# Optimization experiments

Hardware: AMD Instinct MI355X
Metric: run time of the kernel (lower is better)

The kernel has to match this reference:

```python
import jax, jax.numpy as jnp
import numpy as np

N = 150000   # total supergraph nodes (entities+events+chains)
D = 128      # embed_size
H = 4        # attention heads
DH = D // H  # head dim
E = 300000   # edges per layer
L = 4        # layer_specs length
A = 8        # edge attr dim
T = 10       # num_edge_type
TIME_SCALE = 24.0
SLOPE = 0.2  # negative_slope


def setup_inputs() -> dict:
    key = jax.random.key(0)
    ks = jax.random.split(key, 16)
    nrm = lambda k, s, sc=1.0: jax.random.normal(k, s, dtype=jnp.float32) * sc
    return {
        'x': nrm(ks[0], (N, D), 0.1),
        'Wq': nrm(ks[1], (L, D, D), D ** -0.5),
        'Wk': nrm(ks[2], (L, D, D), D ** -0.5),
        'Wv': nrm(ks[3], (L, D, D), D ** -0.5),
        'Wskip': nrm(ks[4], (L, D, D), D ** -0.5),
        'Wa': nrm(ks[5], (L, A, D), 0.1),
        'time_w': nrm(ks[6], (D,)),
        'time_b': nrm(ks[7], (D,), 0.1),
        'dist_w': nrm(ks[8], (D,)),
        'dist_b': nrm(ks[9], (D,), 0.1),
        'type_table': nrm(ks[10], (T, D), 0.1),
        'bn_gamma': jnp.ones((L, D), jnp.float32),
        'bn_beta': jnp.zeros((L, D), jnp.float32),
        'beta': jnp.full((L,), 0.5, jnp.float32),
        'edge_attr': jax.random.uniform(ks[11], (L, E, A), dtype=jnp.float32),
        'edge_dt': jax.random.uniform(ks[12], (L, E), dtype=jnp.float32) * TIME_SCALE,
        'edge_ds': jax.random.uniform(ks[13], (L, E), dtype=jnp.float32) * 10.0,
        'edge_index': jax.random.randint(ks[14], (L, 2, E), 0, N),
        'edge_type': jax.random.randint(ks[15], (L, E), 0, T),
    }


def _layer(x, Wq, Wk, Wv, Wskip, Wa, time_w, time_b, dist_w, dist_b,
           type_table, gamma, bvec, beta, attr, dt, ds, ei, et):
    n = x.shape[0]
    src, dst = ei[0], ei[1]
    # continuous time / distance encoders: cos basis (TimeEncoder / 'time' DistanceEncoder)
    te = jnp.cos((dt / TIME_SCALE)[:, None] * time_w + time_b)   # [E,D]
    de = jnp.cos(ds[:, None] * dist_w + dist_b)                  # [E,D]
    # 'add' edge/time fusion: attr MLP + time + dist + edge-type embeddings
    edge_feat = attr @ Wa + te + de + type_table[et]             # [E,D]
    kv_in = x[src] + edge_feat                                   # gather + fuse
    q = (x @ Wq).reshape(n, H, DH)[dst]                          # [E,H,DH]
    k = (kv_in @ Wk).reshape(-1, H, DH)
    v = (kv_in @ Wv).reshape(-1, H, DH)
    logits = (q * k).sum(-1) * (DH ** -0.5)                      # [E,H]
    logits = jnp.where(logits >= 0, logits, SLOPE * logits)      # leaky_relu(negative_slope)
    # segment softmax over incoming edges of each destination node
    m = jax.ops.segment_max(logits, dst, num_segments=n)
    a = jnp.exp(logits - m[dst])
    denom = jax.ops.segment_sum(a, dst, num_segments=n)
    a = a / denom[dst]
    agg = jax.ops.segment_sum(a[..., None] * v, dst, num_segments=n).reshape(n, D)
    # beta-weighted residual (learn_beta) with skip projection
    out = beta * (x @ Wskip) + (1.0 - beta) * agg
    # BatchNorm1d (training-mode batch stats) + ReLU
    mu = out.mean(0)
    var = out.var(0)
    out = (out - mu) * jax.lax.rsqrt(var + 1e-5) * gamma + bvec
    return jax.nn.relu(out)


def reference(x, Wq, Wk, Wv, Wskip, Wa, time_w, time_b, dist_w, dist_b,
              type_table, bn_gamma, bn_beta, beta, edge_attr, edge_dt,
              edge_ds, edge_index, edge_type):
    for l in range(L):  # entity2event, event2event, event2chain (time filter), chain2chain
        x = _layer(x, Wq[l], Wk[l], Wv[l], Wskip[l], Wa[l],
                   time_w, time_b, dist_w, dist_b, type_table,
                   bn_gamma[l], bn_beta[l], beta[l],
                   edge_attr[l], edge_dt[l], edge_ds[l],
                   edge_index[l], edge_type[l])
    return x
```

## Files before the change

kernel.cpp:

```cpp
#include <hip/hip_runtime.h>

typedef unsigned int u32;
typedef unsigned short u16;
typedef short bf16x8 __attribute__((ext_vector_type(8)));
typedef float f32x4 __attribute__((ext_vector_type(4)));

#define N_NODES 150000
#define E_EDGES 300000
#define L_CNT   151552
#define ETILES  9375
#define NTILES  4688
#define KVBLKS  37500

__device__ __forceinline__ float blo(u32 u){ return __uint_as_float(u << 16); }
__device__ __forceinline__ float bhi(u32 u){ return __uint_as_float(u & 0xffff0000u); }
__device__ __forceinline__ float b2f(u16 h){ return __uint_as_float(((u32)h) << 16); }
__device__ __forceinline__ u16 f2bf(float f){
  u32 u = __float_as_uint(f);
  return (u16)((u + 0x7fffu + ((u >> 16) & 1u)) >> 16);
}
__device__ __forceinline__ u32 pack2(float a, float b){
  return (u32)f2bf(a) | ((u32)f2bf(b) << 16);
}

__device__ __forceinline__ f32x4 mfma16(bf16x8 a, bf16x8 b, f32x4 c){
  return __builtin_amdgcn_mfma_f32_16x16x32_bf16(a, b, c, 0, 0, 0);
}

__device__ __forceinline__ int opsw(int r, int k){ return (r * 128 + k) ^ ((r & 7) << 3); }
__device__ __forceinline__ int csw(int r, int n){ return (r * 128 + n) ^ (((r >> 2) & 3) << 3); }

__global__ __launch_bounds__(256)
void k_wt(const float* __restrict__ Wq, const float* __restrict__ Wk,
          const float* __restrict__ Wv, const float* __restrict__ Ws,
          u16* __restrict__ Wt)
{
  const int m = blockIdx.x;
  const float* src = (m < 4 ? Wq : m < 8 ? Wk : m < 12 ? Wv : Ws)
                     + (size_t)(m & 3) * 16384;
  u16* dst = Wt + (size_t)m * 16384;
  const int t = threadIdx.x;
  for (int i = 0; i < 16; ++i) {
    int idx = i * 256 + t;
    int n = idx >> 5;
    int k4 = (idx & 31) << 2;
    ushort4 o;
    o.x = f2bf(src[(k4 + 0) * 128 + n]);
    o.y = f2bf(src[(k4 + 1) * 128 + n]);
    o.z = f2bf(src[(k4 + 2) * 128 + n]);
    o.w = f2bf(src[(k4 + 3) * 128 + n]);
    *(ushort4*)(dst + n * 128 + k4) = o;
  }
}


__global__ __launch_bounds__(256)
void k_hist(const int* __restrict__ eidx, int* __restrict__ counts)
{
  const int l = blockIdx.y;
  const int e = blockIdx.x * 256 + threadIdx.x;
  if (e < E_EDGES) {
    int dst = eidx[(size_t)l * 2 * E_EDGES + E_EDGES + e];
    atomicAdd(&counts[(size_t)l * L_CNT + dst], 1);
  }
}

__global__ __launch_bounds__(256)
void k_scan1(const int* __restrict__ counts, int* __restrict__ rowptr,
             int* __restrict__ bsum)
{
  __shared__ int sh[256];
  const int b = blockIdx.x, l = blockIdx.y;
  const int t = threadIdx.x;
  const int* c = counts + (size_t)l * L_CNT + b * 2048;
  int* rp = rowptr + (size_t)l * L_CNT + b * 2048;
  int v[8]; int s = 0;
  #pragma unroll
  for (int j = 0; j < 8; ++j) { v[j] = c[t * 8 + j]; s += v[j]; }
  sh[t] = s; __syncthreads();
  for (int off = 1; off < 256; off <<= 1) {
    int x = (t >= off) ? sh[t - off] : 0;
    __syncthreads();
    sh[t] += x;
    __syncthreads();
  }
  int excl = (t == 0) ? 0 : sh[t - 1];
  if (t == 255) bsum[l * 128 + b] = sh[255];
  int run = excl;
  #pragma unroll
  for (int j = 0; j < 8; ++j) { rp[t * 8 + j] = run; run += v[j]; }
}

__global__ __launch_bounds__(128)
void k_scan2(int* __restrict__ bsum)
{
  __shared__ int sh[128];
  const int l = blockIdx.x, t = threadIdx.x;
  int v = (t < 74) ? bsum[l * 128 + t] : 0;
  sh[t] = v; __syncthreads();
  for (int off = 1; off < 128; off <<= 1) {
    int x = (t >= off) ? sh[t - off] : 0;
    __syncthreads();
    sh[t] += x;
    __syncthreads();
  }
  int excl = (t == 0) ? 0 : sh[t - 1];
  if (t < 74) bsum[l * 128 + t] = excl;
}

__global__ __launch_bounds__(256)
void k_scan3(int* __restrict__ rowptr, int* __restrict__ tmp,
             const int* __restrict__ bsum)
{
  const int l = blockIdx.y;
  const int q = blockIdx.x * 256 + threadIdx.x;
  int v = rowptr[(size_t)l * L_CNT + q] + bsum[l * 128 + (q >> 11)];
  rowptr[(size_t)l * L_CNT + q] = v;
  tmp[(size_t)l * L_CNT + q] = v;
}

__global__ __launch_bounds__(256)
void k_scatter(const int* __restrict__ srcP, const int* __restrict__ dstP,
               const int* __restrict__ etP, const float* __restrict__ dtP,
               const float* __restrict__ dsP, const float* __restrict__ attrP,
               int* __restrict__ tmpL, u32* __restrict__ meta)
{
  const int e = blockIdx.x * 256 + threadIdx.x;
  if (e < E_EDGES) {
    int dst = dstP[e];
    int pos = atomicAdd(&tmpL[dst], 1);
    int src = srcP[e];
    int et  = etP[e];
    float dtn = dtP[e] * (1.0f / 24.0f);
    float dsv = dsP[e];
    float4 aA = *(const float4*)(attrP + (size_t)e * 8);
    float4 aB = *(const float4*)(attrP + (size_t)e * 8 + 4);
    uint4 r0, r1;
    r0.x = (u32)src;
    r0.y = (u32)dst | ((u32)et << 20);
    r0.z = __float_as_uint(dtn);
    r0.w = __float_as_uint(dsv);
    r1.x = pack2(aA.x, aA.y); r1.y = pack2(aA.z, aA.w);
    r1.z = pack2(aB.x, aB.y); r1.w = pack2(aB.z, aB.w);
    u32* mp = meta + (size_t)pos * 8;
    *(uint4*)mp = r0;
    *(uint4*)(mp + 4) = r1;
  }
}

__global__ __launch_bounds__(128)
void bn_stats(const float* __restrict__ colsum, const float* __restrict__ colsumsq,
              const float* __restrict__ gamma, const float* __restrict__ bvec,
              float* __restrict__ scsh)
{
  const int d = threadIdx.x;
  const float invN = 1.f / 150000.f;
  float mu = colsum[d] * invN;
  float var = colsumsq[d] * invN - mu * mu;
  float sc = gamma[d] * rsqrtf(var + 1e-5f);
  scsh[d] = sc;
  scsh[128 + d] = bvec[d] - mu * sc;
}


template<int XF32, int BN>
__global__ __launch_bounds__(128, 2)
void prep(const void* __restrict__ xg, const u16* __restrict__ WtQ,
          const u16* __restrict__ WtS, const float* __restrict__ scsh,
          u16* __restrict__ Qo, u16* __restrict__ So,
          const float* __restrict__ Wa, const float* __restrict__ tw,
          const float* __restrict__ tb, const float* __restrict__ dw,
          const float* __restrict__ db, const float* __restrict__ ttab,
          const u32* __restrict__ meta, u16* __restrict__ kvV)
{
  __shared__ __align__(16) u16 As[4160];
  __shared__ __align__(16) u16 Bs[4160];
  const int t = threadIdx.x;

  if (blockIdx.x < NTILES) {
    const int w = t >> 6, lane = t & 63;
    const int lr = lane & 15, hi = lane >> 4;
    const int row0 = blockIdx.x * 32;
    const int nr = min(32, N_NODES - row0);
    const u16* Wt = w ? WtS : WtQ;
    u16* C = w ? So : Qo;

    bf16x8 wt[8][4];
    #pragma unroll
    for (int nb = 0; nb < 8; ++nb)
      #pragma unroll
      for (int ks = 0; ks < 4; ++ks)
        wt[nb][ks] = *(const bf16x8*)(Wt + (nb * 16 + lr) * 128 + ks * 32 + hi * 8);

    #pragma unroll
    for (int i = 0; i < 4; ++i) {
      int idx = i * 128 + t;
      int r = idx >> 4, c8 = (idx & 15) << 3;
      if (r < nr) {
        if (XF32) {
          float4 vA = *(const float4*)((const float*)xg + (size_t)(row0 + r) * 128 + c8);
          float4 vB = *(const float4*)((const float*)xg + (size_t)(row0 + r) * 128 + c8 + 4);
          uint4 o;
          o.x = pack2(vA.x, vA.y); o.y = pack2(vA.z, vA.w);
          o.z = pack2(vB.x, vB.y); o.w = pack2(vB.z, vB.w);
          *(uint4*)(As + opsw(r, c8)) = o;
        } else {
          uint4 v = *(const uint4*)((const u16*)xg + (size_t)(row0 + r) * 128 + c8);
          if (BN) {
            float4 scA = *(const float4*)(scsh + c8);
            float4 scB = *(const float4*)(scsh + c8 + 4);
            float4 shA = *(const float4*)(scsh + 128 + c8);
            float4 shB = *(const float4*)(scsh + 128 + c8 + 4);
            float e0v = fmaxf(fmaf(blo(v.x), scA.x, shA.x), 0.f);
            float e1v = fmaxf(fmaf(bhi(v.x), scA.y, shA.y), 0.f);
            float e2v = fmaxf(fmaf(blo(v.y), scA.z, shA.z), 0.f);
            float e3v = fmaxf(fmaf(bhi(v.y), scA.w, shA.w), 0.f);
            float e4v = fmaxf(fmaf(blo(v.z), scB.x, shB.x), 0.f);
            float e5v = fmaxf(fmaf(bhi(v.z), scB.y, shB.y), 0.f);
            float e6v = fmaxf(fmaf(blo(v.w), scB.z, shB.z), 0.f);
            float e7v = fmaxf(fmaf(bhi(v.w), scB.w, shB.w), 0.f);
            v.x = pack2(e0v, e1v); v.y = pack2(e2v, e3v);
            v.z = pack2(e4v, e5v); v.w = pack2(e6v, e7v);
          }
          *(uint4*)(As + opsw(r, c8)) = v;
        }
      } else {
        *(uint4*)(As + opsw(r, c8)) = make_uint4(0, 0, 0, 0);
      }
    }
    __syncthreads();

    f32x4 acc[2][8];
    #pragma unroll
    for (int a = 0; a < 2; ++a)
      #pragma unroll
      for (int b = 0; b < 8; ++b) {
        acc[a][b][0] = 0.f; acc[a][b][1] = 0.f;
        acc[a][b][2] = 0.f; acc[a][b][3] = 0.f;
      }
    #pragma unroll
    for (int ks = 0; ks < 4; ++ks) {
      const int kb = ks * 32 + hi * 8;
      bf16x8 a0 = *(const bf16x8*)(As + opsw(lr, kb));
      bf16x8 a1 = *(const bf16x8*)(As + opsw(16 + lr, kb));
      #pragma unroll
      for (int nb = 0; nb < 8; ++nb) {
        acc[0][nb] = mfma16(a0, wt[nb][ks], acc[0][nb]);
        acc[1][nb] = mfma16(a1, wt[nb][ks], acc[1][nb]);
      }
    }
    __syncthreads();

    u16* Cs = w ? Bs : As;
    const int g4 = hi << 2;
    #pragma unroll
    for (int mt = 0; mt < 2; ++mt)
      #pragma unroll
      for (int nt = 0; nt < 8; ++nt)
        #pragma unroll
        for (int j = 0; j < 4; ++j)
          Cs[csw(mt * 16 + g4 + j, nt * 16 + lr)] = f2bf(acc[mt][nt][j]);
    #pragma unroll
    for (int i = 0; i < 8; ++i) {
      int idx = i * 64 + lane;
      int r = idx >> 4, n8 = (idx & 15) << 3;
      if (r < nr) {
        uint4 v = *(const uint4*)(Cs + csw(r, n8));
        *(uint4*)(C + (size_t)(row0 + r) * 128 + n8) = v;
      }
    }
  } else {
    const int idx = (blockIdx.x - NTILES) * 128 + t;
    const int e = idx >> 4;
    const int c8 = (idx & 15) << 3;
    const u32* mp = meta + (size_t)e * 8;
    uint4 m0 = *(const uint4*)mp;
    uint4 m1 = *(const uint4*)(mp + 4);
    const int src = (int)m0.x;
    const int et = (int)(m0.y >> 20);
    const float dtn = __uint_as_float(m0.z);
    const float dss = __uint_as_float(m0.w);
    float aa[8] = { blo(m1.x), bhi(m1.x), blo(m1.y), bhi(m1.y),
                    blo(m1.z), bhi(m1.z), blo(m1.w), bhi(m1.w) };
    const float4 twA = *(const float4*)(tw + c8);
    const float4 twB = *(const float4*)(tw + c8 + 4);
    const float4 tbA = *(const float4*)(tb + c8);
    const float4 tbB = *(const float4*)(tb + c8 + 4);
    const float4 dwA = *(const float4*)(dw + c8);
    const float4 dwB = *(const float4*)(dw + c8 + 4);
    const float4 dbA = *(const float4*)(db + c8);
    const float4 dbB = *(const float4*)(db + c8 + 4);
    const float4 ttA = *(const float4*)(ttab + et * 128 + c8);
    const float4 ttB = *(const float4*)(ttab + et * 128 + c8 + 4);
    float f[8];
    f[0] = __cosf(fmaf(dtn, twA.x, tbA.x)) + __cosf(fmaf(dss, dwA.x, dbA.x)) + ttA.x;
    f[1] = __cosf(fmaf(dtn, twA.y, tbA.y)) + __cosf(fmaf(dss, dwA.y, dbA.y)) + ttA.y;
    f[2] = __cosf(fmaf(dtn, twA.z, tbA.z)) + __cosf(fmaf(dss, dwA.z, dbA.z)) + ttA.z;
    f[3] = __cosf(fmaf(dtn, twA.w, tbA.w)) + __cosf(fmaf(dss, dwA.w, dbA.w)) + ttA.w;
    f[4] = __cosf(fmaf(dtn, twB.x, tbB.x)) + __cosf(fmaf(dss, dwB.x, dbB.x)) + ttB.x;
    f[5] = __cosf(fmaf(dtn, twB.y, tbB.y)) + __cosf(fmaf(dss, dwB.y, dbB.y)) + ttB.y;
    f[6] = __cosf(fmaf(dtn, twB.z, tbB.z)) + __cosf(fmaf(dss, dwB.z, dbB.z)) + ttB.z;
    f[7] = __cosf(fmaf(dtn, twB.w, tbB.w)) + __cosf(fmaf(dss, dwB.w, dbB.w)) + ttB.w;
    #pragma unroll
    for (int a = 0; a < 8; ++a) {
      float4 wA = *(const float4*)(Wa + a * 128 + c8);
      float4 wB = *(const float4*)(Wa + a * 128 + c8 + 4);
      f[0] = fmaf(aa[a], wA.x, f[0]);
      f[1] = fmaf(aa[a], wA.y, f[1]);
      f[2] = fmaf(aa[a], wA.z, f[2]);
      f[3] = fmaf(aa[a], wA.w, f[3]);
      f[4] = fmaf(aa[a], wB.x, f[4]);
      f[5] = fmaf(aa[a], wB.y, f[5]);
      f[6] = fmaf(aa[a], wB.z, f[6]);
      f[7] = fmaf(aa[a], wB.w, f[7]);
    }
    float xv[8];
    if (XF32) {
      float4 xA = *(const float4*)((const float*)xg + (size_t)src * 128 + c8);
      float4 xB = *(const float4*)((const float*)xg + (size_t)src * 128 + c8 + 4);
      xv[0] = xA.x; xv[1] = xA.y; xv[2] = xA.z; xv[3] = xA.w;
      xv[4] = xB.x; xv[5] = xB.y; xv[6] = xB.z; xv[7] = xB.w;
    } else {
      uint4 xr = *(const uint4*)((const u16*)xg + (size_t)src * 128 + c8);
      xv[0] = blo(xr.x); xv[1] = bhi(xr.x); xv[2] = blo(xr.y); xv[3] = bhi(xr.y);
      xv[4] = blo(xr.z); xv[5] = bhi(xr.z); xv[6] = blo(xr.w); xv[7] = bhi(xr.w);
    }
    if (BN) {
      float4 scA = *(const float4*)(scsh + c8);
      float4 scB = *(const float4*)(scsh + c8 + 4);
      float4 shA = *(const float4*)(scsh + 128 + c8);
      float4 shB = *(const float4*)(scsh + 128 + c8 + 4);
      xv[0] = fmaxf(fmaf(xv[0], scA.x, shA.x), 0.f);
      xv[1] = fmaxf(fmaf(xv[1], scA.y, shA.y), 0.f);
      xv[2] = fmaxf(fmaf(xv[2], scA.z, shA.z), 0.f);
      xv[3] = fmaxf(fmaf(xv[3], scA.w, shA.w), 0.f);
      xv[4] = fmaxf(fmaf(xv[4], scB.x, shB.x), 0.f);
      xv[5] = fmaxf(fmaf(xv[5], scB.y, shB.y), 0.f);
      xv[6] = fmaxf(fmaf(xv[6], scB.z, shB.z), 0.f);
      xv[7] = fmaxf(fmaf(xv[7], scB.w, shB.w), 0.f);
    }
    uint4 o;
    o.x = pack2(xv[0] + f[0], xv[1] + f[1]);
    o.y = pack2(xv[2] + f[2], xv[3] + f[3]);
    o.z = pack2(xv[4] + f[4], xv[5] + f[5]);
    o.w = pack2(xv[6] + f[6], xv[7] + f[7]);
    *(uint4*)(kvV + (size_t)e * 128 + c8) = o;
  }
}


__global__ __launch_bounds__(128, 2)
void edge_kv(const u16* __restrict__ WtK, const u16* __restrict__ WtV,
             const u32* __restrict__ meta, const u16* __restrict__ Qb,
             u16* __restrict__ kvV, float* __restrict__ logits)
{
  __shared__ __align__(16) u16 KVs[4160];
  __shared__ __align__(16) u16 Qs[4160];
  __shared__ int dstSh[32];
  const int t = threadIdx.x;
  const int w = t >> 6, lane = t & 63;
  const int lr = lane & 15, hi = lane >> 4;
  const int e0 = blockIdx.x * 32;
  const u16* Wt = w ? WtV : WtK;

  bf16x8 wt[8][4];
  #pragma unroll
  for (int nb = 0; nb < 8; ++nb)
    #pragma unroll
    for (int ks = 0; ks < 4; ++ks)
      wt[nb][ks] = *(const bf16x8*)(Wt + (nb * 16 + lr) * 128 + ks * 32 + hi * 8);

  if (w == 0) {
    #pragma unroll
    for (int i = 0; i < 8; ++i) {
      int idx = i * 64 + lane;
      int r = idx >> 4, c8 = (idx & 15) << 3;
      uint4 v = *(const uint4*)(kvV + (size_t)(e0 + r) * 128 + c8);
      *(uint4*)(KVs + opsw(r, c8)) = v;
    }
  } else {
    if (lane < 32)
      dstSh[lane] = (int)(meta[(size_t)(e0 + lane) * 8 + 1] & 0xFFFFFu);
    #pragma unroll
    for (int i = 0; i < 8; ++i) {
      int idx = i * 64 + lane;
      int r = idx >> 4, c8 = (idx & 15) << 3;
      int qrow = dstSh[r];
      uint4 qv = *(const uint4*)(Qb + (size_t)qrow * 128 + c8);
      *(uint4*)(Qs + opsw(r, c8)) = qv;
    }
  }
  __syncthreads();

  if (w == 0) {
    #pragma unroll
    for (int eb = 0; eb < 2; ++eb) {
      f32x4 kacc[8];
      #pragma unroll
      for (int b = 0; b < 8; ++b) {
        kacc[b][0] = 0.f; kacc[b][1] = 0.f; kacc[b][2] = 0.f; kacc[b][3] = 0.f;
      }
      #pragma unroll
      for (int ks = 0; ks < 4; ++ks) {
        bf16x8 ef = *(const bf16x8*)(KVs + opsw(eb * 16 + lr, ks * 32 + hi * 8));
        #pragma unroll
        for (int nb = 0; nb < 8; ++nb)
          kacc[nb] = mfma16(wt[nb][ks], ef, kacc[nb]);
      }
      const int el = eb * 16 + lr;
      float hs[4] = {0.f, 0.f, 0.f, 0.f};
      #pragma unroll
      for (int nb = 0; nb < 8; ++nb) {
        ushort4 q = *(const ushort4*)(Qs + opsw(el, nb * 16 + hi * 4));
        hs[nb >> 1] += b2f(q.x) * kacc[nb][0] + b2f(q.y) * kacc[nb][1]
                     + b2f(q.z) * kacc[nb][2] + b2f(q.w) * kacc[nb][3];
      }
      #pragma unroll
      for (int h = 0; h < 4; ++h) {
        hs[h] += __shfl_xor(hs[h], 16, 64);
        hs[h] += __shfl_xor(hs[h], 32, 64);
        hs[h] *= 0.17677669529663687f;
        hs[h] = (hs[h] >= 0.f) ? hs[h] : 0.2f * hs[h];
      }
      if (lane < 16)
        *(float4*)(logits + (size_t)(e0 + el) * 4) = make_float4(hs[0], hs[1], hs[2], hs[3]);
    }
    __syncthreads();
  } else {
    f32x4 vacc[2][8];
    #pragma unroll
    for (int a = 0; a < 2; ++a)
      #pragma unroll
      for (int b = 0; b < 8; ++b) {
        vacc[a][b][0] = 0.f; vacc[a][b][1] = 0.f;
        vacc[a][b][2] = 0.f; vacc[a][b][3] = 0.f;
      }
    #pragma unroll
    for (int ks = 0; ks < 4; ++ks) {
      const int kb = ks * 32 + hi * 8;
      bf16x8 a0 = *(const bf16x8*)(KVs + opsw(lr, kb));
      bf16x8 a1 = *(const bf16x8*)(KVs + opsw(16 + lr, kb));
      #pragma unroll
      for (int nb = 0; nb < 8; ++nb) {
        vacc[0][nb] = mfma16(a0, wt[nb][ks], vacc[0][nb]);
        vacc[1][nb] = mfma16(a1, wt[nb][ks], vacc[1][nb]);
      }
    }
    __syncthreads();
    const int g4 = hi << 2;
    #pragma unroll
    for (int mt = 0; mt < 2; ++mt)
      #pragma unroll
      for (int nt = 0; nt < 8; ++nt)
        #pragma unroll
        for (int j = 0; j < 4; ++j)
          Qs[csw(mt * 16 + g4 + j, nt * 16 + lr)] = f2bf(vacc[mt][nt][j]);
    #pragma unroll
    for (int i = 0; i < 8; ++i) {
      int idx = i * 64 + lane;
      int r = idx >> 4, n8 = (idx & 15) << 3;
      uint4 v = *(const uint4*)(Qs + csw(r, n8));
      *(uint4*)(kvV + (size_t)(e0 + r) * 128 + n8) = v;
    }
  }
}

template<int PREBF16>
__global__ __launch_bounds__(256)
void node_agg(const u16* __restrict__ Vs, const float* __restrict__ logits,
              const int* __restrict__ rowptr, const u16* __restrict__ S,
              const float* __restrict__ betaP, float* __restrict__ pre,
              u16* __restrict__ preb, float* __restrict__ colsum,
              float* __restrict__ colsumsq)
{
  __shared__ float red[1024];
  const int t = threadIdx.x;
  const int g = t >> 5;
  const int lane = t & 31;
  const int d0 = lane * 4;
  const int h = lane >> 3;
  const float beta = *betaP;
  const float omb = 1.f - beta;
  float s4[4] = {0.f, 0.f, 0.f, 0.f};
  float q4[4] = {0.f, 0.f, 0.f, 0.f};
  for (int rep = 0; rep < 16; ++rep) {
    int n = blockIdx.x * 128 + rep * 8 + g;
    if (n < N_NODES) {
      int rs = rowptr[n], re = rowptr[n + 1];
      float m = -1e30f;
      for (int i = rs; i < re; ++i)
        m = fmaxf(m, logits[(size_t)i * 4 + h]);
      float den = 0.f;
      float a0 = 0.f, a1 = 0.f, a2 = 0.f, a3 = 0.f;
      for (int i = rs; i < re; ++i) {
        float wgt = __expf(logits[(size_t)i * 4 + h] - m);
        den += wgt;
        ushort4 v = *(const ushort4*)(Vs + (size_t)i * 128 + d0);
        a0 = fmaf(wgt, b2f(v.x), a0);
        a1 = fmaf(wgt, b2f(v.y), a1);
        a2 = fmaf(wgt, b2f(v.z), a2);
        a3 = fmaf(wgt, b2f(v.w), a3);
      }
      float inv = (den > 0.f) ? (omb / den) : 0.f;
      ushort4 sv = *(const ushort4*)(S + (size_t)n * 128 + d0);
      float p0 = fmaf(beta, b2f(sv.x), a0 * inv);
      float p1 = fmaf(beta, b2f(sv.y), a1 * inv);
      float p2 = fmaf(beta, b2f(sv.z), a2 * inv);
      float p3 = fmaf(beta, b2f(sv.w), a3 * inv);
      if (PREBF16) {
        ushort4 o;
        o.x = f2bf(p0); o.y = f2bf(p1); o.z = f2bf(p2); o.w = f2bf(p3);
        *(ushort4*)(preb + (size_t)n * 128 + d0) = o;
      } else {
        *(float4*)(pre + (size_t)n * 128 + d0) = make_float4(p0, p1, p2, p3);
      }
      s4[0] += p0; s4[1] += p1; s4[2] += p2; s4[3] += p3;
      q4[0] += p0 * p0; q4[1] += p1 * p1; q4[2] += p2 * p2; q4[3] += p3 * p3;
    }
  }
  *(float4*)(&red[g * 128 + d0]) = make_float4(s4[0], s4[1], s4[2], s4[3]);
  __syncthreads();
  if (t < 128) {
    float tot = 0.f;
    #pragma unroll
    for (int gg = 0; gg < 8; ++gg) tot += red[gg * 128 + t];
    atomicAdd(&colsum[t], tot);
  }
  __syncthreads();
  *(float4*)(&red[g * 128 + d0]) = make_float4(q4[0], q4[1], q4[2], q4[3]);
  __syncthreads();
  if (t < 128) {
    float tot = 0.f;
    #pragma unroll
    for (int gg = 0; gg < 8; ++gg) tot += red[gg * 128 + t];
    atomicAdd(&colsumsq[t], tot);
  }
}

__global__ __launch_bounds__(256)
void bn_apply(const float* __restrict__ pre, const float* __restrict__ colsum,
              const float* __restrict__ colsumsq, const float* __restrict__ gamma,
              const float* __restrict__ bvec, float* __restrict__ outf)
{
  const int idx = blockIdx.x * 256 + threadIdx.x;
  const int n = idx >> 5;
  const int d0 = (idx & 31) * 4;
  const float invN = 1.f / 150000.f;
  float4 p = *(const float4*)(pre + (size_t)n * 128 + d0);
  float4 cs = *(const float4*)(colsum + d0);
  float4 cq = *(const float4*)(colsumsq + d0);
  float4 gm = *(const float4*)(gamma + d0);
  float4 bv = *(const float4*)(bvec + d0);
  float mu, var, y;
  mu = cs.x * invN; var = cq.x * invN - mu * mu;
  y = (p.x - mu) * rsqrtf(var + 1e-5f) * gm.x + bv.x; p.x = fmaxf(y, 0.f);
  mu = cs.y * invN; var = cq.y * invN - mu * mu;
  y = (p.y - mu) * rsqrtf(var + 1e-5f) * gm.y + bv.y; p.y = fmaxf(y, 0.f);
  mu = cs.z * invN; var = cq.z * invN - mu * mu;
  y = (p.z - mu) * rsqrtf(var + 1e-5f) * gm.z + bv.z; p.z = fmaxf(y, 0.f);
  mu = cs.w * invN; var = cq.w * invN - mu * mu;
  y = (p.w - mu) * rsqrtf(var + 1e-5f) * gm.w + bv.w; p.w = fmaxf(y, 0.f);
  *(float4*)(outf + (size_t)n * 128 + d0) = p;
}

extern "C" void kernel_launch(void* const* d_in, const int* in_sizes, int n_in,
                              void* d_out, int out_size, void* d_ws, size_t ws_size,
                              hipStream_t stream)
{
  const float* x0    = (const float*)d_in[0];
  const float* Wq    = (const float*)d_in[1];
  const float* Wk    = (const float*)d_in[2];
  const float* Wv    = (const float*)d_in[3];
  const float* Wsk   = (const float*)d_in[4];
  const float* Wa    = (const float*)d_in[5];
  const float* tw    = (const float*)d_in[6];
  const float* tb    = (const float*)d_in[7];
  const float* dw    = (const float*)d_in[8];
  const float* db    = (const float*)d_in[9];
  const float* ttab  = (const float*)d_in[10];
  const float* gam   = (const float*)d_in[11];
  const float* bet   = (const float*)d_in[12];
  const float* betaP = (const float*)d_in[13];
  const float* attr  = (const float*)d_in[14];
  const float* dt    = (const float*)d_in[15];
  const float* dsv   = (const float*)d_in[16];
  const int*   eidx  = (const int*)d_in[17];
  const int*   etyp  = (const int*)d_in[18];

  char* p = (char*)d_ws;
  u16* xbf  = (u16*)p;       p += 38400000;
  u16* Q    = (u16*)p;       p += 38400000;
  u16* S    = (u16*)p;       p += 38400000;
  u16* kvV  = (u16*)p;       p += 76800000;
  float* logits = (float*)p; p += 4800000;
  int* rowptr = (int*)p;     p += 4 * L_CNT * 4;
  int* tmp    = (int*)p;     p += 4 * L_CNT * 4;
  int* bsum   = (int*)p;     p += 4 * 128 * 4;
  float* colsum   = (float*)p; p += 512;
  float* colsumsq = (float*)p; p += 512;
  float* scsh     = (float*)p; p += 1024;
  u16* Wt = (u16*)p;         p += 16 * 16384 * 2;
  u32* meta = (u32*)p;       p += (size_t)E_EDGES * 32;

  float* pre = (float*)d_out;

  k_wt<<<16, 256, 0, stream>>>(Wq, Wk, Wv, Wsk, Wt);
  hipMemsetAsync(tmp, 0, 4 * L_CNT * 4, stream);
  k_hist<<<dim3(1172, 4), 256, 0, stream>>>(eidx, tmp);
  k_scan1<<<dim3(74, 4), 256, 0, stream>>>(tmp, rowptr, bsum);
  k_scan2<<<4, 128, 0, stream>>>(bsum);
  k_scan3<<<dim3(592, 4), 256, 0, stream>>>(rowptr, tmp, bsum);

  for (int l = 0; l < 4; ++l) {
    const int* srcA = eidx + (size_t)l * 600000;
    const int* dstA = srcA + 300000;
    const int* rpl = rowptr + (size_t)l * L_CNT;
    const u16* WtQl = Wt + (size_t)l * 16384;
    const u16* WtKl = Wt + (size_t)(4 + l) * 16384;
    const u16* WtVl = Wt + (size_t)(8 + l) * 16384;
    const u16* WtSl = Wt + (size_t)(12 + l) * 16384;
    const float* Wal = Wa + (size_t)l * 1024;

    k_scatter<<<1172, 256, 0, stream>>>(
        srcA, dstA, etyp + (size_t)l * 300000, dt + (size_t)l * 300000,
        dsv + (size_t)l * 300000, attr + (size_t)l * 2400000,
        tmp + (size_t)l * L_CNT, meta);

    hipMemsetAsync(colsum, 0, 1024, stream);

    if (l == 0) {
      prep<1, 0><<<NTILES + KVBLKS, 128, 0, stream>>>(
          (const void*)x0, WtQl, WtSl, scsh, Q, S,
          Wal, tw, tb, dw, db, ttab, meta, kvV);
    } else {
      prep<0, 1><<<NTILES + KVBLKS, 128, 0, stream>>>(
          (const void*)xbf, WtQl, WtSl, scsh, Q, S,
          Wal, tw, tb, dw, db, ttab, meta, kvV);
    }

    edge_kv<<<ETILES, 128, 0, stream>>>(WtKl, WtVl, meta, Q, kvV, logits);

    if (l < 3) {
      node_agg<1><<<1172, 256, 0, stream>>>(kvV, logits, rpl, S, betaP + l,
                                            nullptr, xbf, colsum, colsumsq);
      bn_stats<<<1, 128, 0, stream>>>(colsum, colsumsq, gam + (size_t)l * 128,
                                      bet + (size_t)l * 128, scsh);
    } else {
      node_agg<0><<<1172, 256, 0, stream>>>(kvV, logits, rpl, S, betaP + l,
                                            pre, nullptr, colsum, colsumsq);
      bn_apply<<<18750, 256, 0, stream>>>(pre, colsum, colsumsq,
                                          gam + (size_t)l * 128,
                                          bet + (size_t)l * 128, (float*)d_out);
    }
  }
}
```

Measured before the change: 1.429 ms.

## Fuse next-layer edge scatter into prep kernel and interleave GEMM with edge blocks

Removes the per-layer k_scatter launch by appending extra blocks to the prep kernel that build the next layer's CSR-sorted edge metadata into a double-buffered meta array. Only the first layer's scatter is launched separately, before the loop. Prep block indexing now interleaves one node-GEMM tile with every eight edge-feature blocks, so MFMA-heavy and memory-heavy blocks run concurrently instead of in two phases. The cost is a second metadata buffer and a heavier, more branchy prep grid.

```diff
diff --git a/kernel.cpp b/kernel.cpp
--- a/kernel.cpp
+++ b/kernel.cpp
@@ -11,6 +11,8 @@
 #define ETILES  9375
 #define NTILES  4688
 #define KVBLKS  37500
+#define PREPB   42192
+#define SCATB   2344
 
 __device__ __forceinline__ float blo(u32 u){ return __uint_as_float(u << 16); }
 __device__ __forceinline__ float bhi(u32 u){ return __uint_as_float(u & 0xffff0000u); }
@@ -119,6 +121,32 @@
   tmp[(size_t)l * L_CNT + q] = v;
 }
 
+__device__ __forceinline__ void scatter_one(
+    int e, const int* __restrict__ srcP, const int* __restrict__ dstP,
+    const int* __restrict__ etP, const float* __restrict__ dtP,
+    const float* __restrict__ dsP, const float* __restrict__ attrP,
+    int* __restrict__ tmpL, u32* __restrict__ meta)
+{
+  int dst = dstP[e];
+  int pos = atomicAdd(&tmpL[dst], 1);
+  int src = srcP[e];
+  int et  = etP[e];
+  float dtn = dtP[e] * (1.0f / 24.0f);
+  float dsv = dsP[e];
+  float4 aA = *(const float4*)(attrP + (size_t)e * 8);
+  float4 aB = *(const float4*)(attrP + (size_t)e * 8 + 4);
+  uint4 r0, r1;
+  r0.x = (u32)src;
+  r0.y = (u32)dst | ((u32)et << 20);
+  r0.z = __float_as_uint(dtn);
+  r0.w = __float_as_uint(dsv);
+  r1.x = pack2(aA.x, aA.y); r1.y = pack2(aA.z, aA.w);
+  r1.z = pack2(aB.x, aB.y); r1.w = pack2(aB.z, aB.w);
+  u32* mp = meta + (size_t)pos * 8;
+  *(uint4*)mp = r0;
+  *(uint4*)(mp + 4) = r1;
+}
+
 __global__ __launch_bounds__(256)
 void k_scatter(const int* __restrict__ srcP, const int* __restrict__ dstP,
                const int* __restrict__ etP, const float* __restrict__ dtP,
@@ -126,26 +154,8 @@
                int* __restrict__ tmpL, u32* __restrict__ meta)
 {
   const int e = blockIdx.x * 256 + threadIdx.x;
-  if (e < E_EDGES) {
-    int dst = dstP[e];
-    int pos = atomicAdd(&tmpL[dst], 1);
-    int src = srcP[e];
-    int et  = etP[e];
-    float dtn = dtP[e] * (1.0f / 24.0f);
-    float dsv = dsP[e];
-    float4 aA = *(const float4*)(attrP + (size_t)e * 8);
-    float4 aB = *(const float4*)(attrP + (size_t)e * 8 + 4);
-    uint4 r0, r1;
-    r0.x = (u32)src;
-    r0.y = (u32)dst | ((u32)et << 20);
-    r0.z = __float_as_uint(dtn);
-    r0.w = __float_as_uint(dsv);
-    r1.x = pack2(aA.x, aA.y); r1.y = pack2(aA.z, aA.w);
-    r1.z = pack2(aB.x, aB.y); r1.w = pack2(aB.z, aB.w);
-    u32* mp = meta + (size_t)pos * 8;
-    *(uint4*)mp = r0;
-    *(uint4*)(mp + 4) = r1;
-  }
+  if (e < E_EDGES)
+    scatter_one(e, srcP, dstP, etP, dtP, dsP, attrP, tmpL, meta);
 }
 
 __global__ __launch_bounds__(128)
@@ -171,16 +181,28 @@
           const float* __restrict__ Wa, const float* __restrict__ tw,
           const float* __restrict__ tb, const float* __restrict__ dw,
           const float* __restrict__ db, const float* __restrict__ ttab,
-          const u32* __restrict__ meta, u16* __restrict__ kvV)
+          const u32* __restrict__ meta, u16* __restrict__ kvV,
+          const int* __restrict__ srcN, const int* __restrict__ dstN,
+          const int* __restrict__ etN, const float* __restrict__ dtN,
+          const float* __restrict__ dsN, const float* __restrict__ attrN,
+          int* __restrict__ tmpN, u32* __restrict__ metaN)
 {
   __shared__ __align__(16) u16 As[4160];
   __shared__ __align__(16) u16 Bs[4160];
+  const int b = blockIdx.x;
   const int t = threadIdx.x;
 
-  if (blockIdx.x < NTILES) {
+  if (b >= PREPB) {
+    int e = (b - PREPB) * 128 + t;
+    if (metaN != nullptr && e < E_EDGES)
+      scatter_one(e, srcN, dstN, etN, dtN, dsN, attrN, tmpN, metaN);
+    return;
+  }
+
+  if (b % 9 == 0) {
     const int w = t >> 6, lane = t & 63;
     const int lr = lane & 15, hi = lane >> 4;
-    const int row0 = blockIdx.x * 32;
+    const int row0 = (b / 9) * 32;
     const int nr = min(32, N_NODES - row0);
     const u16* Wt = w ? WtS : WtQ;
     u16* C = w ? So : Qo;
@@ -234,9 +256,9 @@
     #pragma unroll
     for (int a = 0; a < 2; ++a)
       #pragma unroll
-      for (int b = 0; b < 8; ++b) {
-        acc[a][b][0] = 0.f; acc[a][b][1] = 0.f;
-        acc[a][b][2] = 0.f; acc[a][b][3] = 0.f;
+      for (int bb = 0; bb < 8; ++bb) {
+        acc[a][bb][0] = 0.f; acc[a][bb][1] = 0.f;
+        acc[a][bb][2] = 0.f; acc[a][bb][3] = 0.f;
       }
     #pragma unroll
     for (int ks = 0; ks < 4; ++ks) {
@@ -270,7 +292,9 @@
       }
     }
   } else {
-    const int idx = (blockIdx.x - NTILES) * 128 + t;
+    const int blk = b - 1 - (b / 9);
+    if (blk >= KVBLKS) return;
+    const int idx = blk * 128 + t;
     const int e = idx >> 4;
     const int c8 = (idx & 15) << 3;
     const u32* mp = meta + (size_t)e * 8;
@@ -600,7 +624,8 @@
   float* colsumsq = (float*)p; p += 512;
   float* scsh     = (float*)p; p += 1024;
   u16* Wt = (u16*)p;         p += 16 * 16384 * 2;
-  u32* meta = (u32*)p;       p += (size_t)E_EDGES * 32;
+  u32* metaA = (u32*)p;      p += (size_t)E_EDGES * 32;
+  u32* metaB = (u32*)p;      p += (size_t)E_EDGES * 32;
 
   float* pre = (float*)d_out;
 
@@ -610,35 +635,48 @@
   k_scan1<<<dim3(74, 4), 256, 0, stream>>>(tmp, rowptr, bsum);
   k_scan2<<<4, 128, 0, stream>>>(bsum);
   k_scan3<<<dim3(592, 4), 256, 0, stream>>>(rowptr, tmp, bsum);
+  k_scatter<<<1172, 256, 0, stream>>>(
+      eidx, eidx + 300000, etyp, dt, dsv, attr, tmp, metaA);
 
   for (int l = 0; l < 4; ++l) {
-    const int* srcA = eidx + (size_t)l * 600000;
-    const int* dstA = srcA + 300000;
     const int* rpl = rowptr + (size_t)l * L_CNT;
     const u16* WtQl = Wt + (size_t)l * 16384;
     const u16* WtKl = Wt + (size_t)(4 + l) * 16384;
     const u16* WtVl = Wt + (size_t)(8 + l) * 16384;
     const u16* WtSl = Wt + (size_t)(12 + l) * 16384;
     const float* Wal = Wa + (size_t)l * 1024;
-
-    k_scatter<<<1172, 256, 0, stream>>>(
-        srcA, dstA, etyp + (size_t)l * 300000, dt + (size_t)l * 300000,
-        dsv + (size_t)l * 300000, attr + (size_t)l * 2400000,
-        tmp + (size_t)l * L_CNT, meta);
+    u32* metaCur = (l & 1) ? metaB : metaA;
+    u32* metaNxt = (l & 1) ? metaA : metaB;
+    const int ln = l + 1;
+    const int* srcN = eidx + (size_t)ln * 600000;
+    const int* dstN = srcN + 300000;
 
     hipMemsetAsync(colsum, 0, 1024, stream);
 
+    const int prepGrid = PREPB + ((l < 3) ? SCATB : 0);
     if (l == 0) {
-      prep<1, 0><<<NTILES + KVBLKS, 128, 0, stream>>>(
+      prep<1, 0><<<prepGrid, 128, 0, stream>>>(
           (const void*)x0, WtQl, WtSl, scsh, Q, S,
-          Wal, tw, tb, dw, db, ttab, meta, kvV);
+          Wal, tw, tb, dw, db, ttab, metaCur, kvV,
+          srcN, dstN, etyp + (size_t)ln * 300000, dt + (size_t)ln * 300000,
+          dsv + (size_t)ln * 300000, attr + (size_t)ln * 2400000,
+          tmp + (size_t)ln * L_CNT, metaNxt);
+    } else if (l < 3) {
+      prep<0, 1><<<prepGrid, 128, 0, stream>>>(
+          (const void*)xbf, WtQl, WtSl, scsh, Q, S,
+          Wal, tw, tb, dw, db, ttab, metaCur, kvV,
+          srcN, dstN, etyp + (size_t)ln * 300000, dt + (size_t)ln * 300000,
+          dsv + (size_t)ln * 300000, attr + (size_t)ln * 2400000,
+          tmp + (size_t)ln * L_CNT, metaNxt);
     } else {
-      prep<0, 1><<<NTILES + KVBLKS, 128, 0, stream>>>(
+      prep<0, 1><<<prepGrid, 128, 0, stream>>>(
           (const void*)xbf, WtQl, WtSl, scsh, Q, S,
-          Wal, tw, tb, dw, db, ttab, meta, kvV);
-    }
-
-    edge_kv<<<ETILES, 128, 0, stream>>>(WtKl, WtVl, meta, Q, kvV, logits);
+          Wal, tw, tb, dw, db, ttab, metaCur, kvV,
+          nullptr, nullptr, nullptr, nullptr, nullptr, nullptr,
+          nullptr, nullptr);
+    }
+
+    edge_kv<<<ETILES, 128, 0, stream>>>(WtKl, WtVl, metaCur, Q, kvV, logits);
 
     if (l < 3) {
       node_agg<1><<<1172, 256, 0, stream>>>(kvV, logits, rpl, S, betaP + l,
```

New measurement: 1.438 ms. About the same (+0.6%).
